# Kernel tuning notes

Hardware: AMD Instinct MI355X
Metric: run time of the kernel (lower is better)

The kernel has to match this reference:

```python
import jax, jax.numpy as jnp
import numpy as np

# FP8 E4M3 format constants
FP8_MAX = 448.0          # largest representable magnitude in E4M3
MANT_BITS = 3            # mantissa bits
_TINY = 2.0 ** -24


def fp8_fake_quant(x):
    """Per-tensor dynamic-scale FP8 (E4M3) fake quantization with STE.

    amax tracking (single-entry history on first call) -> scale = FP8_MAX/amax,
    scale, clamp to format range, round mantissa to MANT_BITS, dequantize.
    """
    amax = jax.lax.stop_gradient(jnp.max(jnp.abs(x)))
    scale = FP8_MAX / jnp.maximum(amax, _TINY)
    xs = jnp.clip(x * scale, -FP8_MAX, FP8_MAX)
    a = jnp.abs(xs)
    # exponent of each value; floor(log2) gives the binade, lsb is the quantum
    e = jnp.floor(jnp.log2(jnp.maximum(a, _TINY)))
    lsb = jnp.exp2(e - MANT_BITS)
    q = jnp.round(xs / lsb) * lsb
    q = jnp.where(a == 0.0, 0.0, q) / scale
    # straight-through estimator: forward q, backward identity
    return x + jax.lax.stop_gradient(q - x)


def setup_inputs() -> dict:
    key = jax.random.key(0)
    k1, k2, k3 = jax.random.split(key, 3)
    tokens, d_in, d_out = 4096, 4096, 16384
    x = jax.random.normal(k1, (tokens, d_in), dtype=jnp.float32)
    weight = jax.random.normal(k2, (d_out, d_in), dtype=jnp.float32) * 0.02
    bias = jax.random.normal(k3, (d_out,), dtype=jnp.float32) * 0.02
    return {"x": x, "weight": weight, "bias": bias}


def reference(x, weight, bias):
    qw = fp8_fake_quant(weight)          # quantize weights
    qx = fp8_fake_quant(x)               # quantize_input=True
    # F.linear: x @ W^T + b
    return jnp.einsum("ti,oi->to", qx, qw) + bias
```

## Files before the change

kernel.cpp:

```cpp
#include <hip/hip_runtime.h>
#include <hip/hip_bf16.h>


typedef __attribute__((ext_vector_type(8))) __bf16 bf16x8;
typedef __attribute__((ext_vector_type(4))) float f32x4;
typedef __attribute__((ext_vector_type(4))) unsigned int u32x4;

#define FP8_MAX 448.0f
#define TINY 5.9604644775390625e-8f

__device__ __forceinline__ void gload_lds16(const void* g, void* l) {
  __builtin_amdgcn_global_load_lds(
      (__attribute__((address_space(1))) void*)g,
      (__attribute__((address_space(3))) void*)l, 16, 0, 0);
}

__global__ __launch_bounds__(256) void amax_kernel(
    const float* __restrict__ in, long n, unsigned* __restrict__ out) {
  long i0 = (long)blockIdx.x * blockDim.x + threadIdx.x;
  long stride = (long)gridDim.x * blockDim.x;
  long n4 = n >> 2;
  const float4* in4 = (const float4*)in;
  float m = 0.f;
  for (long i = i0; i < n4; i += stride) {
    float4 v = in4[i];
    m = fmaxf(m, fmaxf(fmaxf(fabsf(v.x), fabsf(v.y)),
                       fmaxf(fabsf(v.z), fabsf(v.w))));
  }
  #pragma unroll
  for (int off = 32; off > 0; off >>= 1)
    m = fmaxf(m, __shfl_xor(m, off, 64));
  __shared__ float red[4];
  int lane = threadIdx.x & 63, wid = threadIdx.x >> 6;
  if (lane == 0) red[wid] = m;
  __syncthreads();
  if (threadIdx.x == 0) {
    m = fmaxf(fmaxf(red[0], red[1]), fmaxf(red[2], red[3]));
    atomicMax(out, __float_as_uint(m));
  }
}

__device__ __forceinline__ unsigned short fq1(float x, float s) {
  float xs = x * s;
  xs = fminf(fmaxf(xs, -FP8_MAX), FP8_MAX);
  unsigned u = __float_as_uint(xs);
  unsigned sign = u & 0x80000000u;
  unsigned mag = u & 0x7fffffffu;
  unsigned r = (mag + 0x7FFFFu + ((mag >> 20) & 1u)) & 0xFFF00000u;
  return (unsigned short)((sign | r) >> 16);
}

__global__ __launch_bounds__(256) void quant_kernel(
    const float* __restrict__ in, unsigned short* __restrict__ out,
    const unsigned* __restrict__ amaxp, long n) {
  float s = FP8_MAX / fmaxf(__uint_as_float(*amaxp), TINY);
  long i0 = (long)blockIdx.x * blockDim.x + threadIdx.x;
  long stride = (long)gridDim.x * blockDim.x;
  long n4 = n >> 2;
  const float4* in4 = (const float4*)in;
  uint2* out4 = (uint2*)out;
  for (long i = i0; i < n4; i += stride) {
    float4 v = in4[i];
    unsigned a = fq1(v.x, s), b = fq1(v.y, s), c = fq1(v.z, s), d = fq1(v.w, s);
    uint2 o;
    o.x = a | (b << 16);
    o.y = c | (d << 16);
    out4[i] = o;
  }
}

__global__ __launch_bounds__(256, 2) void gemm_kernel(
    const unsigned short* __restrict__ qx, const unsigned short* __restrict__ qw,
    const float* __restrict__ bias, const unsigned* __restrict__ amaxp,
    float* __restrict__ out, int M, int N, int K) {
  __shared__ unsigned short As[128 * 64];
  __shared__ unsigned short Bs[128 * 64];
  const int tid = threadIdx.x;
  const int lane = tid & 63;
  const int wid = tid >> 6;
  const int wm = wid >> 1, wn = wid & 1;
  const int bm0 = blockIdx.y * 128;
  const int bn0 = blockIdx.x * 128;

  f32x4 acc[4][4] = {};

  const int arow = wm * 64 + (lane & 15);
  const int brow = wn * 64 + (lane & 15);
  const int koff = (lane >> 4) << 3;

  for (int kt = 0; kt < K; kt += 64) {
    #pragma unroll
    for (int i = 0; i < 4; ++i) {
      int off = i * 4096 + wid * 1024 + lane * 16;
      int r = off >> 7;
      int c = off & 127;
      gload_lds16((const char*)qx + (((size_t)(bm0 + r) * K + kt) << 1) + c,
                  (char*)As + i * 4096 + wid * 1024);
      gload_lds16((const char*)qw + (((size_t)(bn0 + r) * K + kt) << 1) + c,
                  (char*)Bs + i * 4096 + wid * 1024);
    }
    __syncthreads();
    #pragma unroll
    for (int kk = 0; kk < 2; ++kk) {
      bf16x8 af[4], bfr[4];
      #pragma unroll
      for (int t = 0; t < 4; ++t) {
        af[t] = __builtin_bit_cast(
            bf16x8, *(const u32x4*)&As[(arow + t * 16) * 64 + kk * 32 + koff]);
        bfr[t] = __builtin_bit_cast(
            bf16x8, *(const u32x4*)&Bs[(brow + t * 16) * 64 + kk * 32 + koff]);
      }
      #pragma unroll
      for (int mt = 0; mt < 4; ++mt)
        #pragma unroll
        for (int nt = 0; nt < 4; ++nt)
          acc[mt][nt] = __builtin_amdgcn_mfma_f32_16x16x32_bf16(
              af[mt], bfr[nt], acc[mt][nt], 0, 0, 0);
    }
    __syncthreads();
  }

  const float ax = fmaxf(__uint_as_float(amaxp[0]), TINY);
  const float aw = fmaxf(__uint_as_float(amaxp[1]), TINY);
  const float inv = ax * aw * (1.0f / (FP8_MAX * FP8_MAX));
  const int col0 = bn0 + wn * 64 + (lane & 15);
  const int row0 = bm0 + wm * 64 + ((lane >> 4) << 2);
  float bv[4];
  #pragma unroll
  for (int nt = 0; nt < 4; ++nt) bv[nt] = bias[col0 + nt * 16];
  #pragma unroll
  for (int mt = 0; mt < 4; ++mt)
    #pragma unroll
    for (int nt = 0; nt < 4; ++nt)
      #pragma unroll
      for (int j = 0; j < 4; ++j)
        out[(size_t)(row0 + mt * 16 + j) * N + col0 + nt * 16] =
            acc[mt][nt][j] * inv + bv[nt];
}

extern "C" void kernel_launch(void* const* d_in, const int* in_sizes, int n_in,
                              void* d_out, int out_size, void* d_ws, size_t ws_size,
                              hipStream_t stream) {
  const float* x = (const float*)d_in[0];
  const float* w = (const float*)d_in[1];
  const float* bias = (const float*)d_in[2];
  float* out = (float*)d_out;

  long nx = in_sizes[0];
  long nw = in_sizes[1];
  int N = in_sizes[2];
  int K = (int)(nw / N);
  int M = (int)(nx / K);

  unsigned* amax = (unsigned*)d_ws;
  unsigned short* qx = (unsigned short*)((char*)d_ws + 256);
  unsigned short* qw = (unsigned short*)((char*)d_ws + 256 + (size_t)M * K * 2);

  hipMemsetAsync(d_ws, 0, 256, stream);
  amax_kernel<<<2048, 256, 0, stream>>>(x, nx, amax + 0);
  amax_kernel<<<2048, 256, 0, stream>>>(w, nw, amax + 1);
  quant_kernel<<<2048, 256, 0, stream>>>(x, qx, amax + 0, nx);
  quant_kernel<<<2048, 256, 0, stream>>>(w, qw, amax + 1, nw);

  dim3 grid(N / 128, M / 128);
  gemm_kernel<<<grid, 256, 0, stream>>>(qx, qw, bias, amax, out, M, N, K);
}
```

Measured before the change: 1.199 ms.

## Rework bf16 GEMM with 256x256 tiles, double-buffered LDS, swizzle and grid remap

The GEMM moves to 512-thread blocks computing 256x256 output tiles (8x4 MFMA tiles per wave), raising arithmetic intensity per LDS load. Loads for the next k-tile are staged into a second LDS buffer while the current one is consumed, split into two k-halves with partial vmcnt waits. LDS columns are XOR-swizzled to avoid bank conflicts, MFMA runs at raised priority, and a 1D grid with an XCD-aware block remap improves L2 locality. The quant kernel writes 16-byte vectors. The cost is 128 KB of LDS and heavy register pressure from 128 accumulator floats per thread, which may limit occupancy or cause spills.

After: 1.210 ms. No clear change (+0.9%).

```diff
diff --git a/kernel.cpp b/kernel.cpp
--- a/kernel.cpp
+++ b/kernel.cpp
@@ -40,14 +40,14 @@
   }
 }
 
-__device__ __forceinline__ unsigned short fq1(float x, float s) {
+__device__ __forceinline__ unsigned fq1(float x, float s) {
   float xs = x * s;
   xs = fminf(fmaxf(xs, -FP8_MAX), FP8_MAX);
   unsigned u = __float_as_uint(xs);
   unsigned sign = u & 0x80000000u;
   unsigned mag = u & 0x7fffffffu;
   unsigned r = (mag + 0x7FFFFu + ((mag >> 20) & 1u)) & 0xFFF00000u;
-  return (unsigned short)((sign | r) >> 16);
+  return (sign | r) >> 16;
 }
 
 __global__ __launch_bounds__(256) void quant_kernel(
@@ -56,86 +56,122 @@
   float s = FP8_MAX / fmaxf(__uint_as_float(*amaxp), TINY);
   long i0 = (long)blockIdx.x * blockDim.x + threadIdx.x;
   long stride = (long)gridDim.x * blockDim.x;
-  long n4 = n >> 2;
+  long n8 = n >> 3;
   const float4* in4 = (const float4*)in;
-  uint2* out4 = (uint2*)out;
-  for (long i = i0; i < n4; i += stride) {
-    float4 v = in4[i];
-    unsigned a = fq1(v.x, s), b = fq1(v.y, s), c = fq1(v.z, s), d = fq1(v.w, s);
-    uint2 o;
-    o.x = a | (b << 16);
-    o.y = c | (d << 16);
-    out4[i] = o;
-  }
-}
-
-__global__ __launch_bounds__(256, 2) void gemm_kernel(
+  u32x4* out8 = (u32x4*)out;
+  for (long i = i0; i < n8; i += stride) {
+    float4 v0 = in4[2 * i];
+    float4 v1 = in4[2 * i + 1];
+    u32x4 o;
+    o.x = fq1(v0.x, s) | (fq1(v0.y, s) << 16);
+    o.y = fq1(v0.z, s) | (fq1(v0.w, s) << 16);
+    o.z = fq1(v1.x, s) | (fq1(v1.y, s) << 16);
+    o.w = fq1(v1.z, s) | (fq1(v1.w, s) << 16);
+    out8[i] = o;
+  }
+}
+
+__global__ __launch_bounds__(512, 2) void gemm_kernel(
     const unsigned short* __restrict__ qx, const unsigned short* __restrict__ qw,
     const float* __restrict__ bias, const unsigned* __restrict__ amaxp,
     float* __restrict__ out, int M, int N, int K) {
-  __shared__ unsigned short As[128 * 64];
-  __shared__ unsigned short Bs[128 * 64];
+  __shared__ unsigned short As[2][2][256 * 32];
+  __shared__ unsigned short Bs[2][2][256 * 32];
+
   const int tid = threadIdx.x;
   const int lane = tid & 63;
   const int wid = tid >> 6;
-  const int wm = wid >> 1, wn = wid & 1;
-  const int bm0 = blockIdx.y * 128;
-  const int bn0 = blockIdx.x * 128;
-
-  f32x4 acc[4][4] = {};
-
-  const int arow = wm * 64 + (lane & 15);
-  const int brow = wn * 64 + (lane & 15);
-  const int koff = (lane >> 4) << 3;
-
-  for (int kt = 0; kt < K; kt += 64) {
-    #pragma unroll
-    for (int i = 0; i < 4; ++i) {
-      int off = i * 4096 + wid * 1024 + lane * 16;
-      int r = off >> 7;
-      int c = off & 127;
-      gload_lds16((const char*)qx + (((size_t)(bm0 + r) * K + kt) << 1) + c,
-                  (char*)As + i * 4096 + wid * 1024);
-      gload_lds16((const char*)qw + (((size_t)(bn0 + r) * K + kt) << 1) + c,
-                  (char*)Bs + i * 4096 + wid * 1024);
-    }
-    __syncthreads();
-    #pragma unroll
-    for (int kk = 0; kk < 2; ++kk) {
-      bf16x8 af[4], bfr[4];
-      #pragma unroll
-      for (int t = 0; t < 4; ++t) {
-        af[t] = __builtin_bit_cast(
-            bf16x8, *(const u32x4*)&As[(arow + t * 16) * 64 + kk * 32 + koff]);
-        bfr[t] = __builtin_bit_cast(
-            bf16x8, *(const u32x4*)&Bs[(brow + t * 16) * 64 + kk * 32 + koff]);
-      }
-      #pragma unroll
-      for (int mt = 0; mt < 4; ++mt)
-        #pragma unroll
-        for (int nt = 0; nt < 4; ++nt)
-          acc[mt][nt] = __builtin_amdgcn_mfma_f32_16x16x32_bf16(
-              af[mt], bfr[nt], acc[mt][nt], 0, 0, 0);
-    }
-    __syncthreads();
+  const int wr = wid >> 2;
+  const int wc = wid & 3;
+
+  const int nbn = N >> 8;
+  const int cpx = gridDim.x >> 3;
+  const int swz = (blockIdx.x & 7) * cpx + (blockIdx.x >> 3);
+  const int bm0 = (swz / nbn) << 8;
+  const int bn0 = (swz % nbn) << 8;
+
+  f32x4 acc[8][4] = {};
+
+  const int srow = tid >> 2;
+  const int scb = ((tid & 3) * 16) ^ ((srow & 3) << 4);
+  const size_t a_off = (size_t)(bm0 + srow) * K + (scb >> 1);
+  const size_t b_off = (size_t)(bn0 + srow) * K + (scb >> 1);
+  const size_t jstride = (size_t)128 * K;
+  const int ldsb = wid * 1024;
+
+  const int rcb = (((lane >> 4) << 4) ^ ((lane & 3) << 4)) >> 1;
+  const int arb = (wr * 128 + (lane & 15)) * 32 + rcb;
+  const int brb = (wc * 64 + (lane & 15)) * 32 + rcb;
+
+#define STAGE(d, kh, kt)                                                   \
+  {                                                                        \
+    const unsigned short* ga = qx + a_off + (kt) + (kh) * 32;              \
+    const unsigned short* gb = qw + b_off + (kt) + (kh) * 32;              \
+    char* la = (char*)&As[d][kh][0] + ldsb;                                \
+    char* lb = (char*)&Bs[d][kh][0] + ldsb;                                \
+    gload_lds16(ga, la);                                                   \
+    gload_lds16(ga + jstride, la + 8192);                                  \
+    gload_lds16(gb, lb);                                                   \
+    gload_lds16(gb + jstride, lb + 8192);                                  \
+  }
+
+#define PHASE(d, kh)                                                       \
+  {                                                                        \
+    bf16x8 a[8], b[4];                                                     \
+    _Pragma("unroll")                                                      \
+    for (int m = 0; m < 8; ++m)                                            \
+      a[m] = __builtin_bit_cast(bf16x8,                                    \
+                *(const u32x4*)&As[d][kh][arb + m * 512]);                 \
+    _Pragma("unroll")                                                      \
+    for (int n = 0; n < 4; ++n)                                            \
+      b[n] = __builtin_bit_cast(bf16x8,                                    \
+                *(const u32x4*)&Bs[d][kh][brb + n * 512]);                 \
+    __builtin_amdgcn_s_setprio(1);                                         \
+    _Pragma("unroll")                                                      \
+    for (int m = 0; m < 8; ++m)                                            \
+      _Pragma("unroll")                                                    \
+      for (int n = 0; n < 4; ++n)                                          \
+        acc[m][n] = __builtin_amdgcn_mfma_f32_16x16x32_bf16(               \
+            a[m], b[n], acc[m][n], 0, 0, 0);                               \
+    __builtin_amdgcn_s_setprio(0);                                         \
+  }
+
+  STAGE(0, 0, 0);
+  STAGE(0, 1, 0);
+
+  const int nt = K >> 6;
+  int cur = 0;
+  for (int t = 0; t < nt; ++t) {
+    const int ktn = (t + 1 == nt) ? 0 : ((t + 1) << 6);
+    STAGE(cur ^ 1, 0, ktn);
+    asm volatile("s_waitcnt vmcnt(8)" ::: "memory");
+    __builtin_amdgcn_s_barrier();
+    PHASE(cur, 0);
+    STAGE(cur ^ 1, 1, ktn);
+    asm volatile("s_waitcnt vmcnt(8)" ::: "memory");
+    __builtin_amdgcn_s_barrier();
+    PHASE(cur, 1);
+    __builtin_amdgcn_s_barrier();
+    cur ^= 1;
   }
 
   const float ax = fmaxf(__uint_as_float(amaxp[0]), TINY);
   const float aw = fmaxf(__uint_as_float(amaxp[1]), TINY);
   const float inv = ax * aw * (1.0f / (FP8_MAX * FP8_MAX));
-  const int col0 = bn0 + wn * 64 + (lane & 15);
-  const int row0 = bm0 + wm * 64 + ((lane >> 4) << 2);
-  float bv[4];
+  const int col0 = bn0 + wc * 64 + (lane & 15);
+  const int row0 = bm0 + wr * 128 + ((lane >> 4) << 2);
   #pragma unroll
-  for (int nt = 0; nt < 4; ++nt) bv[nt] = bias[col0 + nt * 16];
-  #pragma unroll
-  for (int mt = 0; mt < 4; ++mt)
+  for (int n = 0; n < 4; ++n) {
+    float bv = bias[col0 + n * 16];
     #pragma unroll
-    for (int nt = 0; nt < 4; ++nt)
+    for (int m = 0; m < 8; ++m)
       #pragma unroll
       for (int j = 0; j < 4; ++j)
-        out[(size_t)(row0 + mt * 16 + j) * N + col0 + nt * 16] =
-            acc[mt][nt][j] * inv + bv[nt];
+        out[(size_t)(row0 + m * 16 + j) * N + col0 + n * 16] =
+            acc[m][n][j] * inv + bv;
+  }
+#undef STAGE
+#undef PHASE
 }
 
 extern "C" void kernel_launch(void* const* d_in, const int* in_sizes, int n_in,
@@ -159,9 +195,9 @@
   hipMemsetAsync(d_ws, 0, 256, stream);
   amax_kernel<<<2048, 256, 0, stream>>>(x, nx, amax + 0);
   amax_kernel<<<2048, 256, 0, stream>>>(w, nw, amax + 1);
-  quant_kernel<<<2048, 256, 0, stream>>>(x, qx, amax + 0, nx);
-  quant_kernel<<<2048, 256, 0, stream>>>(w, qw, amax + 1, nw);
-
-  dim3 grid(N / 128, M / 128);
-  gemm_kernel<<<grid, 256, 0, stream>>>(qx, qw, bias, amax, out, M, N, K);
-}
+  quant_kernel<<<4096, 256, 0, stream>>>(x, qx, amax + 0, nx);
+  quant_kernel<<<4096, 256, 0, stream>>>(w, qw, amax + 1, nw);
+
+  int nwg = (M >> 8) * (N >> 8);
+  gemm_kernel<<<nwg, 512, 0, stream>>>(qx, qw, bias, amax, out, M, N, K);
+}
```
